# Optimization experiments

Measured on AMD Instinct MI355X. Metric: run time of the kernel, lower is better.

The kernel has to match this reference:

```python
import jax, jax.numpy as jnp
import numpy as np

FILTER_SZ = 5  # matches init_kwargs filter_sz


def setup_inputs() -> dict:
    key = jax.random.key(0)
    image = jax.random.normal(key, (16, 3, 512, 512), dtype=jnp.float32)
    return {"image": image}


def reference(image):
    # scipy.ndimage.median_filter with default mode='reflect' ((d c b a | a b c d)),
    # which corresponds to jnp.pad mode='symmetric'.
    k = FILTER_SZ
    pad = k // 2
    B, C, H, W = image.shape
    padded = jnp.pad(image, ((0, 0), (0, 0), (pad, pad), (pad, pad)), mode="symmetric")
    # Gather all k*k shifted views: [B, C, H, W, k*k]. Fixed small loop over the
    # window offsets (k*k = 25), fully vectorized over batch/channel/spatial dims.
    patches = jnp.stack(
        [padded[:, :, i:i + H, j:j + W] for i in range(k) for j in range(k)],
        axis=-1,
    )
    # Order statistic: median of the k*k window per pixel.
    return jnp.median(patches, axis=-1)
```

## Files before the change

### kernel.cpp

```cpp
#include <hip/hip_runtime.h>


typedef _Float16 h2 __attribute__((ext_vector_type(2)));

static __device__ __forceinline__ h2 h2min(h2 a, h2 b) { return __builtin_elementwise_min(a, b); }
static __device__ __forceinline__ h2 h2max(h2 a, h2 b) { return __builtin_elementwise_max(a, b); }

static __device__ __forceinline__ h2 pack2(float a, float b) {
    return __builtin_bit_cast(h2, __builtin_amdgcn_cvt_pkrtz(a, b));
}

#define CAS(a, b) do { h2 _mn = h2min((a), (b)); (b) = h2max((a), (b)); (a) = _mn; } while (0)

static __device__ __forceinline__ h2 med3h(h2 a, h2 b, h2 c) {
    return h2max(h2min(a, b), h2min(h2max(a, b), c));
}

static __device__ __forceinline__ h2 sel7of13_ds(h2 d0, h2 e0, h2 c1, h2 d1, h2 e1,
                                                 h2 b2, h2 c2, h2 d2,
                                                 h2 a3, h2 b3, h2 c3, h2 a4, h2 b4) {
    CAS(c1, b2); CAS(d0, c1); CAS(e1, d2);
    h2 w0 = a3, w1 = b3, w2 = e0, w3 = c1, w4 = d1, w5 = e1, w6 = b2, w7 = c2;
    CAS(w2, w3); CAS(w4, w5); CAS(w6, w7);
    CAS(w0, w2); CAS(w4, w6); CAS(w0, w4);
    CAS(w1, w3); CAS(w5, w7); CAS(w3, w7);
    h2 v0 = a4, v1 = b4, v2 = w1, v3 = w2, v4 = w3, v5 = w4, v6 = w5, v7 = w6;
    CAS(v2, v3); CAS(v4, v5); CAS(v6, v7);
    CAS(v0, v2); CAS(v4, v6); CAS(v0, v4);
    CAS(v1, v3); CAS(v5, v7); CAS(v3, v7);
    h2 u0 = v1, u1 = v2, u2 = v3, u3 = v4, u4 = v5, u5 = v6;
    CAS(u0, u1); CAS(u2, u3); CAS(u4, u5);
    CAS(u0, u2); CAS(u0, u4);
    CAS(u1, u3); CAS(u3, u5);
    h2 t1 = h2min(u1, u2), t2 = h2max(u1, u2);
    h2 t3 = h2min(u3, u4), t4 = h2max(u3, u4);
    return med3h(h2max(t1, t3), h2min(t2, t4), c3);
}

static __device__ __forceinline__ int refl(int v, int n) {
    v = (v < 0) ? (-v - 1) : v;
    return (v >= n) ? (2 * n - 1 - v) : v;
}

constexpr int W = 512, H = 512, R = 8, PX = 4;

__global__ __launch_bounds__(256) void median5x5_kernel(const float* __restrict__ in,
                                                        float* __restrict__ out) {
    const int tx = blockIdx.x * 64 + threadIdx.x;
    const int x0 = PX * tx;
    const int ystrip = blockIdx.y * 4 + threadIdx.y;
    const int y0 = ystrip * R;
    const size_t plane = (size_t)blockIdx.z * ((size_t)H * W);
    const float* __restrict__ p = in + plane;
    float* __restrict__ q = out + plane;

    const bool swapA = (x0 == 0);
    const bool swapD = (x0 == W - PX);
    const int aB = swapA ? 0 : x0 - 2;
    const int dB = swapD ? x0 + 2 : x0 + 4;

    auto load_raw = [&](int y, float (&f)[8]) {
        const float* __restrict__ rp = p + (size_t)refl(y, H) * W;
        float2 a = *reinterpret_cast<const float2*>(rp + aB);
        float2 b = *reinterpret_cast<const float2*>(rp + x0);
        float2 c = *reinterpret_cast<const float2*>(rp + (x0 + 2));
        float2 d = *reinterpret_cast<const float2*>(rp + dB);
        f[0] = swapA ? a.y : a.x;
        f[1] = swapA ? a.x : a.y;
        f[2] = b.x; f[3] = b.y; f[4] = c.x; f[5] = c.y;
        f[6] = swapD ? d.y : d.x;
        f[7] = swapD ? d.x : d.y;
    };

    auto pack_sort2 = [&](h2 (&dA)[5], h2 (&dB_)[5], const float (&f)[8]) {
        h2 w1 = pack2(f[1], f[2]);
        h2 w2 = pack2(f[2], f[3]);
        h2 w3 = pack2(f[3], f[4]);
        h2 w4 = pack2(f[4], f[5]);
        CAS(w2, w3); CAS(w2, w4); CAS(w3, w4);
        dA[0] = pack2(f[0], f[1]); dA[1] = w1; dA[2] = w2; dA[3] = w3; dA[4] = w4;
        CAS(dA[0], dA[1]); CAS(dA[0], dA[3]); CAS(dA[0], dA[2]);
        CAS(dA[1], dA[4]); CAS(dA[1], dA[3]); CAS(dA[1], dA[2]);
        dB_[0] = pack2(f[5], f[6]); dB_[1] = pack2(f[6], f[7]);
        dB_[2] = w2; dB_[3] = w3; dB_[4] = w4;
        CAS(dB_[0], dB_[1]); CAS(dB_[0], dB_[3]); CAS(dB_[0], dB_[2]);
        CAS(dB_[1], dB_[4]); CAS(dB_[1], dB_[3]); CAS(dB_[1], dB_[2]);
    };

    auto ins_top2 = [&](h2 g2, h2 g3, h2 x, h2 &p3, h2 &p4) {
        h2 u3 = h2min(g3, x); p4 = h2max(g3, x); p3 = h2max(g2, u3);
    };
    auto ins_top3 = [&](h2 g1, h2 g2, h2 g3, h2 x, h2 &p2, h2 &p3, h2 &p4) {
        h2 u3 = h2min(g3, x); p4 = h2max(g3, x); p3 = h2max(g2, u3);
        h2 u2 = h2min(g2, u3); p2 = h2max(g1, u2);
    };
    auto ins_mid3 = [&](h2 g0, h2 g1, h2 g2, h2 g3, h2 x, h2 &p1, h2 &p2, h2 &p3) {
        h2 u3 = h2min(g3, x); p3 = h2max(g2, u3);
        h2 u2 = h2min(g2, u3); p2 = h2max(g1, u2);
        h2 u1 = h2min(g1, u2); p1 = h2max(g0, u1);
    };
    auto ins_bot3 = [&](h2 g0, h2 g1, h2 g2, h2 x, h2 &p0, h2 &p1, h2 &p2) {
        p0 = h2min(g0, x); h2 t1 = h2max(g0, x);
        p1 = h2min(g1, t1); h2 t2 = h2max(g1, t1);
        p2 = h2min(g2, t2);
    };
    auto ins_bot2 = [&](h2 g0, h2 g1, h2 x, h2 &p0, h2 &p1) {
        p0 = h2min(g0, x); p1 = h2min(g1, h2max(g0, x));
    };

    auto pair_medians = [&](h2 (&s0)[5], h2 (&s1)[5], h2 (&s2)[5], h2 (&s3)[5],
                            h2 (&s4)[5], h2 (&s5)[5], h2 &mT, h2 &mU) {
        h2 Td0,Te0,Tc1,Td1,Te1,Tb2,Tc2,Td2,Ta3,Tb3,Tc3,Ta4,Tb4;
        h2 Ud0,Ue0,Uc1,Ud1,Ue1,Ub2,Uc2,Ud2,Ua3,Ub3,Uc3,Ua4,Ub4;
        {
            h2 g0=s1[0], g1=s2[0], g2=s3[0], g3=s4[0];
            CAS(g0,g1); CAS(g2,g3); CAS(g0,g2); CAS(g1,g3); CAS(g1,g2);
            ins_top2(g2, g3, s0[0], Ta3, Ta4);
            ins_top2(g2, g3, s5[0], Ua3, Ua4);
            (void)g0;
        }
        {
            h2 g0=s1[1], g1=s2[1], g2=s3[1], g3=s4[1];
            CAS(g0,g1); CAS(g2,g3); CAS(g0,g2); CAS(g1,g3); CAS(g1,g2);
            ins_top3(g1, g2, g3, s0[1], Tb2, Tb3, Tb4);
            ins_top3(g1, g2, g3, s5[1], Ub2, Ub3, Ub4);
            (void)g0;
        }
        {
            h2 g0=s1[2], g1=s2[2], g2=s3[2], g3=s4[2];
            CAS(g0,g1); CAS(g2,g3); CAS(g0,g2); CAS(g1,g3); CAS(g1,g2);
            ins_mid3(g0, g1, g2, g3, s0[2], Tc1, Tc2, Tc3);
            ins_mid3(g0, g1, g2, g3, s5[2], Uc1, Uc2, Uc3);
        }
        {
            h2 g0=s1[3], g1=s2[3], g2=s3[3], g3=s4[3];
            CAS(g0,g1); CAS(g2,g3); CAS(g0,g2); CAS(g1,g3); CAS(g1,g2);
            ins_bot3(g0, g1, g2, s0[3], Td0, Td1, Td2);
            ins_bot3(g0, g1, g2, s5[3], Ud0, Ud1, Ud2);
            (void)g3;
        }
        {
            h2 g0=s1[4], g1=s2[4], g2=s3[4], g3=s4[4];
            CAS(g0,g1); CAS(g2,g3); CAS(g0,g2); CAS(g1,g3); CAS(g1,g2);
            ins_bot2(g0, g1, s0[4], Te0, Te1);
            ins_bot2(g0, g1, s5[4], Ue0, Ue1);
            (void)g2; (void)g3;
        }
        mT = sel7of13_ds(Td0,Te0,Tc1,Td1,Te1,Tb2,Tc2,Td2,Ta3,Tb3,Tc3,Ta4,Tb4);
        mU = sel7of13_ds(Ud0,Ue0,Uc1,Ud1,Ue1,Ub2,Uc2,Ud2,Ua3,Ub3,Uc3,Ua4,Ub4);
    };

    h2 rowsA[6][5], rowsB[6][5];

    #pragma unroll
    for (int k = 0; k < 4; ++k) {
        float f[8];
        load_raw(y0 - 2 + k, f);
        pack_sort2(rowsA[k], rowsB[k], f);
    }

    float cfA[8], cfB[8];
    load_raw(y0 + 2, cfA);
    load_raw(y0 + 3, cfB);

    #pragma unroll
    for (int i = 0; i < 4; ++i) {
        const int cur = y0 + 2 * i;
        pack_sort2(rowsA[(2*i + 4) % 6], rowsB[(2*i + 4) % 6], cfA);
        if (i < 3) load_raw(cur + 4, cfA);
        pack_sort2(rowsA[(2*i + 5) % 6], rowsB[(2*i + 5) % 6], cfB);
        if (i < 3) load_raw(cur + 5, cfB);

        h2 mA0, mA1, mB0, mB1;
        pair_medians(rowsA[(2*i + 0) % 6], rowsA[(2*i + 1) % 6], rowsA[(2*i + 2) % 6],
                     rowsA[(2*i + 3) % 6], rowsA[(2*i + 4) % 6], rowsA[(2*i + 5) % 6],
                     mA0, mA1);
        pair_medians(rowsB[(2*i + 0) % 6], rowsB[(2*i + 1) % 6], rowsB[(2*i + 2) % 6],
                     rowsB[(2*i + 3) % 6], rowsB[(2*i + 4) % 6], rowsB[(2*i + 5) % 6],
                     mB0, mB1);

        float4 o0, o1;
        o0.x = (float)mA0.x; o0.y = (float)mA0.y;
        o0.z = (float)mB0.x; o0.w = (float)mB0.y;
        o1.x = (float)mA1.x; o1.y = (float)mA1.y;
        o1.z = (float)mB1.x; o1.w = (float)mB1.y;
        *reinterpret_cast<float4*>(q + (size_t)cur * W + x0) = o0;
        *reinterpret_cast<float4*>(q + (size_t)(cur + 1) * W + x0) = o1;
    }
}

extern "C" void kernel_launch(void* const* d_in, const int* in_sizes, int n_in,
                              void* d_out, int out_size, void* d_ws, size_t ws_size,
                              hipStream_t stream) {
    const float* in = (const float*)d_in[0];
    float* out = (float*)d_out;
    dim3 block(64, 4, 1);
    dim3 grid(512 / (64 * PX), 512 / (4 * R), 16 * 3);
    hipLaunchKernelGGL(median5x5_kernel, grid, block, 0, stream, in, out);
}
```

Before: 110.9 us.

## Halve per-thread column width to two pixels with single packed row sort

Each thread now covers 2 columns instead of 4. It loads 6 floats per row instead of 8 and does one full 5-element packed sort per row, with no longer any shared 3-element pre-sort reused across two halves. The grid doubles in x to raise thread count and parallelism and to lower register pressure. In exchange it gives up horizontal reuse across the two halves, so each output pixel costs more comparisons and more loads, and stores shrink to float2.

```diff
diff --git a/kernel.cpp b/kernel.cpp
--- a/kernel.cpp
+++ b/kernel.cpp
@@ -11,6 +11,11 @@
 }
 
 #define CAS(a, b) do { h2 _mn = h2min((a), (b)); (b) = h2max((a), (b)); (a) = _mn; } while (0)
+
+static __device__ __forceinline__ void sort5(h2 &e0, h2 &e1, h2 &e2, h2 &e3, h2 &e4) {
+    CAS(e0, e1); CAS(e3, e4); CAS(e2, e4); CAS(e2, e3); CAS(e0, e3);
+    CAS(e0, e2); CAS(e1, e4); CAS(e1, e3); CAS(e1, e2);
+}
 
 static __device__ __forceinline__ h2 med3h(h2 a, h2 b, h2 c) {
     return h2max(h2min(a, b), h2min(h2max(a, b), c));
@@ -42,7 +47,7 @@
     return (v >= n) ? (2 * n - 1 - v) : v;
 }
 
-constexpr int W = 512, H = 512, R = 8, PX = 4;
+constexpr int W = 512, H = 512, R = 8, PX = 2;
 
 __global__ __launch_bounds__(256) void median5x5_kernel(const float* __restrict__ in,
                                                         float* __restrict__ out) {
@@ -57,34 +62,27 @@
     const bool swapA = (x0 == 0);
     const bool swapD = (x0 == W - PX);
     const int aB = swapA ? 0 : x0 - 2;
-    const int dB = swapD ? x0 + 2 : x0 + 4;
+    const int dB = swapD ? x0 : x0 + 2;
 
-    auto load_raw = [&](int y, float (&f)[8]) {
+    auto load_raw = [&](int y, float (&f)[6]) {
         const float* __restrict__ rp = p + (size_t)refl(y, H) * W;
         float2 a = *reinterpret_cast<const float2*>(rp + aB);
         float2 b = *reinterpret_cast<const float2*>(rp + x0);
-        float2 c = *reinterpret_cast<const float2*>(rp + (x0 + 2));
-        float2 d = *reinterpret_cast<const float2*>(rp + dB);
+        float2 c = *reinterpret_cast<const float2*>(rp + dB);
         f[0] = swapA ? a.y : a.x;
         f[1] = swapA ? a.x : a.y;
-        f[2] = b.x; f[3] = b.y; f[4] = c.x; f[5] = c.y;
-        f[6] = swapD ? d.y : d.x;
-        f[7] = swapD ? d.x : d.y;
+        f[2] = b.x; f[3] = b.y;
+        f[4] = swapD ? c.y : c.x;
+        f[5] = swapD ? c.x : c.y;
     };
 
-    auto pack_sort2 = [&](h2 (&dA)[5], h2 (&dB_)[5], const float (&f)[8]) {
-        h2 w1 = pack2(f[1], f[2]);
-        h2 w2 = pack2(f[2], f[3]);
-        h2 w3 = pack2(f[3], f[4]);
-        h2 w4 = pack2(f[4], f[5]);
-        CAS(w2, w3); CAS(w2, w4); CAS(w3, w4);
-        dA[0] = pack2(f[0], f[1]); dA[1] = w1; dA[2] = w2; dA[3] = w3; dA[4] = w4;
-        CAS(dA[0], dA[1]); CAS(dA[0], dA[3]); CAS(dA[0], dA[2]);
-        CAS(dA[1], dA[4]); CAS(dA[1], dA[3]); CAS(dA[1], dA[2]);
-        dB_[0] = pack2(f[5], f[6]); dB_[1] = pack2(f[6], f[7]);
-        dB_[2] = w2; dB_[3] = w3; dB_[4] = w4;
-        CAS(dB_[0], dB_[1]); CAS(dB_[0], dB_[3]); CAS(dB_[0], dB_[2]);
-        CAS(dB_[1], dB_[4]); CAS(dB_[1], dB_[3]); CAS(dB_[1], dB_[2]);
+    auto pack_sort = [&](h2 (&d)[5], const float (&f)[6]) {
+        d[0] = pack2(f[0], f[1]);
+        d[1] = pack2(f[1], f[2]);
+        d[2] = pack2(f[2], f[3]);
+        d[3] = pack2(f[3], f[4]);
+        d[4] = pack2(f[4], f[5]);
+        sort5(d[0], d[1], d[2], d[3], d[4]);
     };
 
     auto ins_top2 = [&](h2 g2, h2 g3, h2 x, h2 &p3, h2 &p4) {
@@ -150,42 +148,37 @@
         mU = sel7of13_ds(Ud0,Ue0,Uc1,Ud1,Ue1,Ub2,Uc2,Ud2,Ua3,Ub3,Uc3,Ua4,Ub4);
     };
 
-    h2 rowsA[6][5], rowsB[6][5];
+    h2 rows[6][5];
 
     #pragma unroll
     for (int k = 0; k < 4; ++k) {
-        float f[8];
+        float f[6];
         load_raw(y0 - 2 + k, f);
-        pack_sort2(rowsA[k], rowsB[k], f);
+        pack_sort(rows[k], f);
     }
 
-    float cfA[8], cfB[8];
+    float cfA[6], cfB[6];
     load_raw(y0 + 2, cfA);
     load_raw(y0 + 3, cfB);
 
     #pragma unroll
-    for (int i = 0; i < 4; ++i) {
+    for (int i = 0; i < R / 2; ++i) {
         const int cur = y0 + 2 * i;
-        pack_sort2(rowsA[(2*i + 4) % 6], rowsB[(2*i + 4) % 6], cfA);
-        if (i < 3) load_raw(cur + 4, cfA);
-        pack_sort2(rowsA[(2*i + 5) % 6], rowsB[(2*i + 5) % 6], cfB);
-        if (i < 3) load_raw(cur + 5, cfB);
+        pack_sort(rows[(2*i + 4) % 6], cfA);
+        if (i < R / 2 - 1) load_raw(cur + 4, cfA);
+        pack_sort(rows[(2*i + 5) % 6], cfB);
+        if (i < R / 2 - 1) load_raw(cur + 5, cfB);
 
-        h2 mA0, mA1, mB0, mB1;
-        pair_medians(rowsA[(2*i + 0) % 6], rowsA[(2*i + 1) % 6], rowsA[(2*i + 2) % 6],
-                     rowsA[(2*i + 3) % 6], rowsA[(2*i + 4) % 6], rowsA[(2*i + 5) % 6],
-                     mA0, mA1);
-        pair_medians(rowsB[(2*i + 0) % 6], rowsB[(2*i + 1) % 6], rowsB[(2*i + 2) % 6],
-                     rowsB[(2*i + 3) % 6], rowsB[(2*i + 4) % 6], rowsB[(2*i + 5) % 6],
-                     mB0, mB1);
+        h2 m0, m1;
+        pair_medians(rows[(2*i + 0) % 6], rows[(2*i + 1) % 6], rows[(2*i + 2) % 6],
+                     rows[(2*i + 3) % 6], rows[(2*i + 4) % 6], rows[(2*i + 5) % 6],
+                     m0, m1);
 
-        float4 o0, o1;
-        o0.x = (float)mA0.x; o0.y = (float)mA0.y;
-        o0.z = (float)mB0.x; o0.w = (float)mB0.y;
-        o1.x = (float)mA1.x; o1.y = (float)mA1.y;
-        o1.z = (float)mB1.x; o1.w = (float)mB1.y;
-        *reinterpret_cast<float4*>(q + (size_t)cur * W + x0) = o0;
-        *reinterpret_cast<float4*>(q + (size_t)(cur + 1) * W + x0) = o1;
+        float2 o0, o1;
+        o0.x = (float)m0.x; o0.y = (float)m0.y;
+        o1.x = (float)m1.x; o1.y = (float)m1.y;
+        *reinterpret_cast<float2*>(q + (size_t)cur * W + x0) = o0;
+        *reinterpret_cast<float2*>(q + (size_t)(cur + 1) * W + x0) = o1;
     }
 }
 
```

Measured after the change: 114.4 us. 1.03x slower.
